# Performance work log

Measured on AMD Instinct MI355X. Metric: run time of the kernel, lower is better.

Reference implementation:

```python
import jax, jax.numpy as jnp
import numpy as np

DIM = 64
B, H, W = 4, 80, 80


def setup_inputs() -> dict:
    key = jax.random.key(0)
    k1, k2, k3 = jax.random.split(key, 3)
    x = jax.random.normal(k1, (B, DIM, H, W), dtype=jnp.float32)
    # 1x1 conv == per-pixel linear: weight [3*dim, dim], bias [3*dim]
    w_qkv = jax.random.normal(k2, (3 * DIM, DIM), dtype=jnp.float32) * (1.0 / np.sqrt(DIM).astype(np.float32))
    b_qkv = jax.random.normal(k3, (3 * DIM,), dtype=jnp.float32) * 0.01
    return {"x": x, "w_qkv": w_qkv, "b_qkv": b_qkv}


def reference(x, w_qkv, b_qkv):
    Bb, C, Hh, Ww = x.shape
    N = Hh * Ww
    # 1x1 conv -> qkv, chunked along channels
    qkv = jnp.einsum('bchw,oc->bohw', x, w_qkv) + b_qkv[None, :, None, None]
    q, k, v = jnp.split(qkv, 3, axis=1)  # each [B,C,H,W]

    # --- spatial attention (uses q on both sides, as in the original) ---
    # qk: transpose(3,1) -> [B,W,H,C] -> [B, W*H, C]
    qk = jnp.transpose(q, (0, 3, 2, 1)).reshape(Bb, N, C)
    # kq: [B, C, H*W]  (note: different flatten order than qk, faithful to source)
    kq = q.reshape(Bb, C, N)
    ms = jax.nn.softmax(jnp.matmul(qk, kq), axis=-1)  # [B, N, N]

    # --- channel attention ---
    kf = k.reshape(Bb, C, N)                                # [B, C, N]
    qf = jnp.transpose(q, (0, 3, 2, 1)).reshape(Bb, N, C)   # [B, N, C]
    ma = jax.nn.softmax(jnp.matmul(kf, qf), axis=-1)        # [B, C, C]

    # --- apply to v ---
    vq = jnp.transpose(v, (0, 3, 2, 1)).reshape(Bb, N, C)   # [B, N, C]
    ms_out = jnp.matmul(ms, vq)                             # [B, N, C]
    ms_out = jnp.swapaxes(ms_out, 1, 2).reshape(Bb, C, Hh, Ww)
    ma_out = jnp.matmul(ma, v.reshape(Bb, C, N)).reshape(Bb, C, Hh, Ww)
    return ms_out + ma_out
```

## Files before the change

kernel.cpp:

```cpp
#include <hip/hip_runtime.h>
#include <stdint.h>

#define BATCH 4
#define CH 64
#define HW 80
#define NPIX 6400
#define SPLITS 3

typedef __attribute__((ext_vector_type(8))) short bf16x8;
typedef __attribute__((ext_vector_type(4))) float f32x4;

#define QSCALE 1.2011224087864498f
#define ESHIFT 115.41560327111707f

static __device__ __forceinline__ unsigned short f2bf(float f) {
  union { float f; unsigned int u; } v; v.f = f;
  unsigned int u = v.u;
  return (unsigned short)((u + 0x7fffu + ((u >> 16) & 1u)) >> 16);
}
static __device__ __forceinline__ float bf2f(unsigned short h) {
  union { unsigned int u; float f; } v; v.u = ((unsigned int)h) << 16;
  return v.f;
}
static __device__ __forceinline__ unsigned int split_pack(float a) {
  unsigned short hi = f2bf(a);
  union { unsigned int u; float f; } hf; hf.u = ((unsigned int)hi) << 16;
  unsigned short lo = f2bf(a - hf.f);
  return (unsigned int)hi | ((unsigned int)lo << 16);
}
static __device__ __forceinline__ void deint(uint4 a, uint4 b, bf16x8* h, bf16x8* l) {
  union { unsigned int u[4]; bf16x8 v; } H, L;
  H.u[0] = __builtin_amdgcn_perm(a.y, a.x, 0x05040100u);
  H.u[1] = __builtin_amdgcn_perm(a.w, a.z, 0x05040100u);
  H.u[2] = __builtin_amdgcn_perm(b.y, b.x, 0x05040100u);
  H.u[3] = __builtin_amdgcn_perm(b.w, b.z, 0x05040100u);
  L.u[0] = __builtin_amdgcn_perm(a.y, a.x, 0x07060302u);
  L.u[1] = __builtin_amdgcn_perm(a.w, a.z, 0x07060302u);
  L.u[2] = __builtin_amdgcn_perm(b.y, b.x, 0x07060302u);
  L.u[3] = __builtin_amdgcn_perm(b.w, b.z, 0x07060302u);
  *h = H.v; *l = L.v;
}
static __device__ __forceinline__ void gload16(const unsigned short* g, char* l) {
  __builtin_amdgcn_global_load_lds(
      (const __attribute__((address_space(1))) unsigned int*)(g),
      (__attribute__((address_space(3))) unsigned int*)(l), 16, 0, 0);
}

__global__ __launch_bounds__(512) void qkv_kernel(
    const float* __restrict__ x, const float* __restrict__ w,
    const float* __restrict__ bias, unsigned short* __restrict__ Qtbf,
    unsigned short* __restrict__ Vbf, unsigned int* __restrict__ Kpk,
    unsigned int* __restrict__ Qtn) {
  __shared__ float qs[64][65];
  int bid = blockIdx.x;
  int b = bid / 100, tile = bid % 100;
  int p0 = tile * 64;
  int t = threadIdx.x;
  int i = t & 63;
  int og = __builtin_amdgcn_readfirstlane(t >> 6);
  int p = p0 + i;
  int tp = (p % HW) * HW + p / HW;
  const float* xb = x + (size_t)b * CH * NPIX + p;
  float xv[64];
#pragma unroll
  for (int c = 0; c < 64; ++c) xv[c] = xb[(size_t)c * NPIX];
  size_t bc = (size_t)b * CH * NPIX;
  for (int j = 0; j < 24; j += 4) {
    int o = og * 24 + j;
    const float* wr0 = w + o * 64;
    const float* wr1 = wr0 + 64;
    const float* wr2 = wr0 + 128;
    const float* wr3 = wr0 + 192;
    float a0 = bias[o], a1 = bias[o + 1], a2 = bias[o + 2], a3 = bias[o + 3];
#pragma unroll
    for (int c = 0; c < 64; ++c) {
      float xc = xv[c];
      a0 += wr0[c] * xc;
      a1 += wr1[c] * xc;
      a2 += wr2[c] * xc;
      a3 += wr3[c] * xc;
    }
    float av[4] = {a0, a1, a2, a3};
#pragma unroll
    for (int u = 0; u < 4; ++u) {
      int oo = o + u;
      int cc = oo & 63;
      int kind = oo >> 6;
      float a = av[u];
      if (kind == 0) {
        qs[cc][i] = a;
        Qtn[bc + (size_t)cc * NPIX + tp] = split_pack(a);
      } else if (kind == 1) {
        Kpk[bc + (size_t)cc * NPIX + p] = split_pack(a);
      } else {
        Vbf[bc + (size_t)cc * NPIX + p] = f2bf(a);
      }
    }
  }
  __syncthreads();
  int j2 = t >> 3, g = t & 7;
  int pj = p0 + j2;
  int tpj = (pj % HW) * HW + pj / HW;
  unsigned int pk4[4];
#pragma unroll
  for (int q4 = 0; q4 < 4; ++q4) {
    float a0 = qs[g * 8 + q4 * 2][j2] * QSCALE;
    float a1 = qs[g * 8 + q4 * 2 + 1][j2] * QSCALE;
    pk4[q4] = (unsigned int)f2bf(a0) | ((unsigned int)f2bf(a1) << 16);
  }
  unsigned short* dst = Qtbf + ((size_t)b * NPIX + tpj) * 64 + g * 8;
  uint4 w0 = {pk4[0], pk4[1], pk4[2], pk4[3]};
  *(uint4*)&dst[0] = w0;
}

__global__ __launch_bounds__(256) void gram_kernel(
    const unsigned int* __restrict__ Kpk, const unsigned int* __restrict__ Qtn,
    float* __restrict__ Pc) {
  int bid = blockIdx.x;
  int b = bid / 200, chunk = bid % 200;
  int n0 = chunk * 32;
  int t = threadIdx.x;
  int w = t >> 6, lane = t & 63;
  int quad = lane >> 4, l16 = lane & 15;
  size_t bc = (size_t)b * CH * NPIX;

  f32x4 acc[4];
#pragma unroll
  for (int ct = 0; ct < 4; ++ct) acc[ct] = (f32x4){0.f, 0.f, 0.f, 0.f};

  const unsigned int* kp = Kpk + bc + (size_t)(w * 16 + l16) * NPIX + n0;
  uint4 ua = *(const uint4*)&kp[quad * 8];
  uint4 ub = *(const uint4*)&kp[quad * 8 + 4];
  bf16x8 ah, al;
  deint(ua, ub, &ah, &al);
#pragma unroll
  for (int ct = 0; ct < 4; ++ct) {
    const unsigned int* qp = Qtn + bc + (size_t)(ct * 16 + l16) * NPIX + n0;
    uint4 va = *(const uint4*)&qp[quad * 8];
    uint4 vb = *(const uint4*)&qp[quad * 8 + 4];
    bf16x8 bh, bl;
    deint(va, vb, &bh, &bl);
    acc[ct] = __builtin_amdgcn_mfma_f32_16x16x32_bf16(ah, bh, acc[ct], 0, 0, 0);
    acc[ct] = __builtin_amdgcn_mfma_f32_16x16x32_bf16(ah, bl, acc[ct], 0, 0, 0);
    acc[ct] = __builtin_amdgcn_mfma_f32_16x16x32_bf16(al, bh, acc[ct], 0, 0, 0);
  }
#pragma unroll
  for (int ct = 0; ct < 4; ++ct)
#pragma unroll
    for (int r = 0; r < 4; ++r)
      atomicAdd(&Pc[((size_t)b * 64 + w * 16 + quad * 4 + r) * 64 + ct * 16 + l16],
                acc[ct][r]);
}

__global__ __launch_bounds__(256) void flash_kernel(
    const unsigned short* __restrict__ Qtbf, const unsigned short* __restrict__ Vbf,
    float* __restrict__ Opart, float* __restrict__ Lpart) {
  __shared__ char smem[40960] __attribute__((aligned(128)));

  int bid = blockIdx.x;
  int b = bid / 300;
  int rem = bid % 300;
  int qt = rem / 3, split = rem % 3;
  int p0 = qt * 64;
  int t = threadIdx.x;
  int w = t >> 6, lane = t & 63;
  int quad = lane >> 4, l16 = lane & 15;
  int sw = l16 & 7;
  size_t bq = (size_t)b * NPIX;
  size_t bC = (size_t)b * CH * NPIX;

  bf16x8 aq[2];
#pragma unroll
  for (int ks = 0; ks < 2; ++ks)
    aq[ks] = *(const bf16x8*)&Qtbf[(bq + p0 + w * 16 + l16) * 64 + ks * 32 + quad * 8];

  f32x4 oacc[4];
#pragma unroll
  for (int ct = 0; ct < 4; ++ct) oacc[ct] = (f32x4){0.f, 0.f, 0.f, 0.f};
  float psum = 0.f;

  const unsigned short* Kb = Qtbf + bq * 64;
  const unsigned short* Vb = Vbf + bC;

  int lr = lane >> 3, ls = lane & 7;
  int colsw = (ls ^ lr) * 8;
  int rA = w * 8 + lr;
  int rB = 32 + w * 8 + lr;
  int ldsA = __builtin_amdgcn_readfirstlane(w * 1024);
  int ldsB = ldsA + 4096;

  int kt0 = split * 34;
  int niter = (split == 2) ? 32 : 34;

  const unsigned short* gKA = Kb + (size_t)(kt0 * 64 + rA) * 64 + colsw;
  const unsigned short* gKB = Kb + (size_t)(kt0 * 64 + rB) * 64 + colsw;
  const unsigned short* gVA = Vb + (size_t)rA * NPIX + kt0 * 64 + colsw;
  const unsigned short* gVB = Vb + (size_t)rB * NPIX + kt0 * 64 + colsw;

  gload16(gKA, smem + ldsA);
  gload16(gKB, smem + ldsB);
  gload16(gVA, smem + 16384 + ldsA);
  gload16(gVB, smem + 16384 + ldsB);
  gKA += 64 * 64; gKB += 64 * 64; gVA += 64; gVB += 64;
  __syncthreads();

  unsigned short* Pw = (unsigned short*)(smem + 32768) + w * 16 * 64;
  for (int it = 0; it < niter; ++it) {
    int cur = it & 1;
    if (it + 1 < niter) {
      int off = (cur ^ 1) << 13;
      gload16(gKA, smem + off + ldsA);
      gload16(gKB, smem + off + ldsB);
      gload16(gVA, smem + 16384 + off + ldsA);
      gload16(gVB, smem + 16384 + off + ldsB);
      gKA += 64 * 64; gKB += 64 * 64; gVA += 64; gVB += 64;
    }
    unsigned short* Ksc = (unsigned short*)(smem + (cur << 13));
    unsigned short* Vsc = (unsigned short*)(smem + 16384 + (cur << 13));
    f32x4 sc[4];
#pragma unroll
    for (int ct = 0; ct < 4; ++ct)
      sc[ct] = (f32x4){-ESHIFT, -ESHIFT, -ESHIFT, -ESHIFT};
    __builtin_amdgcn_s_setprio(1);
#pragma unroll
    for (int ks = 0; ks < 2; ++ks)
#pragma unroll
      for (int ct = 0; ct < 4; ++ct) {
        bf16x8 bk = *(const bf16x8*)&Ksc[(ct * 16 + l16) * 64 +
                                         (((ks * 4 + quad) ^ sw) << 3)];
        sc[ct] = __builtin_amdgcn_mfma_f32_16x16x32_bf16(bk, aq[ks], sc[ct], 0, 0, 0);
      }
    __builtin_amdgcn_s_setprio(0);
#pragma unroll
    for (int ct = 0; ct < 4; ++ct) {
      float e0 = __builtin_amdgcn_exp2f(sc[ct][0]);
      float e1 = __builtin_amdgcn_exp2f(sc[ct][1]);
      float e2 = __builtin_amdgcn_exp2f(sc[ct][2]);
      float e3 = __builtin_amdgcn_exp2f(sc[ct][3]);
      psum += (e0 + e1) + (e2 + e3);
      unsigned int pk0, pk1;
      asm("v_cvt_pk_bf16_f32 %0, %1, %2" : "=v"(pk0) : "v"(e0), "v"(e1));
      asm("v_cvt_pk_bf16_f32 %0, %1, %2" : "=v"(pk1) : "v"(e2), "v"(e3));
      uint2 pk = {pk0, pk1};
      *(uint2*)&Pw[l16 * 64 +
                   (((2 * ct + (quad >> 1)) ^ sw) << 3) + ((quad & 1) << 2)] = pk;
    }
    bf16x8 pf[2];
#pragma unroll
    for (int ks = 0; ks < 2; ++ks)
      pf[ks] = *(const bf16x8*)&Pw[l16 * 64 + (((ks * 4 + quad) ^ sw) << 3)];
    __builtin_amdgcn_s_setprio(1);
#pragma unroll
    for (int ks = 0; ks < 2; ++ks)
#pragma unroll
      for (int ct = 0; ct < 4; ++ct) {
        bf16x8 vf = *(const bf16x8*)&Vsc[(ct * 16 + l16) * 64 +
                                         (((ks * 4 + quad) ^ sw) << 3)];
        oacc[ct] = __builtin_amdgcn_mfma_f32_16x16x32_bf16(vf, pf[ks], oacc[ct], 0, 0, 0);
      }
    __builtin_amdgcn_s_setprio(0);
    __syncthreads();
  }
  float* Op = Opart + (size_t)(split * BATCH + b) * CH * NPIX;
  int pcol = p0 + w * 16 + l16;
  {
    float s = psum;
    s += __shfl_xor(s, 16, 64);
    s += __shfl_xor(s, 32, 64);
    if (quad == 0) Lpart[(size_t)(split * BATCH + b) * NPIX + pcol] = s;
  }
#pragma unroll
  for (int ct = 0; ct < 4; ++ct)
#pragma unroll
    for (int r = 0; r < 4; ++r)
      Op[(size_t)(ct * 16 + quad * 4 + r) * NPIX + pcol] = oacc[ct][r];
}

__global__ __launch_bounds__(256) void finalize_kernel(
    const float* __restrict__ Pc, const unsigned short* __restrict__ Vbf,
    const float* __restrict__ Opart, const float* __restrict__ Lpart,
    float* __restrict__ out) {
  __shared__ float maT[64 * 64];
  int bid = blockIdx.x;
  int b = bid / 100, nt = bid % 100;
  int t = threadIdx.x;
  if (t < 64) {
    int c = t;
    const float* row = Pc + ((size_t)b * 64 + c) * 64;
    float v[64];
    float mx = -1e30f;
#pragma unroll
    for (int j = 0; j < 64; ++j) { v[j] = row[j]; mx = fmaxf(mx, v[j]); }
    float s = 0.f;
#pragma unroll
    for (int j = 0; j < 64; ++j) { v[j] = __expf(v[j] - mx); s += v[j]; }
    float inv = 1.f / s;
#pragma unroll
    for (int j = 0; j < 64; ++j) maT[j * 64 + c] = v[j] * inv;
  }
  __syncthreads();
  int lane = t & 63, ct = t >> 6;
  int n = nt * 64 + lane;
  size_t bc = (size_t)b * CH * NPIX;
  const unsigned short* vb = Vbf + bc + n;
  float acc[16];
#pragma unroll
  for (int j = 0; j < 16; ++j) acc[j] = 0.f;
  for (int cp = 0; cp < 64; ++cp) {
    float vv = bf2f(vb[(size_t)cp * NPIX]);
    const float* m = &maT[cp * 64 + ct * 16];
    f32x4 m0 = *(const f32x4*)&m[0];
    f32x4 m1 = *(const f32x4*)&m[4];
    f32x4 m2 = *(const f32x4*)&m[8];
    f32x4 m3 = *(const f32x4*)&m[12];
#pragma unroll
    for (int j = 0; j < 4; ++j) {
      acc[j] += m0[j] * vv;
      acc[4 + j] += m1[j] * vv;
      acc[8 + j] += m2[j] * vv;
      acc[12 + j] += m3[j] * vv;
    }
  }
  float lsum = Lpart[(size_t)(0 * BATCH + b) * NPIX + n] +
               Lpart[(size_t)(1 * BATCH + b) * NPIX + n] +
               Lpart[(size_t)(2 * BATCH + b) * NPIX + n];
  float inv = 1.f / lsum;
  const float* O0 = Opart + (size_t)(0 * BATCH + b) * CH * NPIX;
  const float* O1 = Opart + (size_t)(1 * BATCH + b) * CH * NPIX;
  const float* O2 = Opart + (size_t)(2 * BATCH + b) * CH * NPIX;
#pragma unroll
  for (int j = 0; j < 16; ++j) {
    size_t co = (size_t)(ct * 16 + j) * NPIX + n;
    float o = O0[co] + O1[co] + O2[co];
    out[bc + co] = acc[j] + o * inv;
  }
}

extern "C" void kernel_launch(void* const* d_in, const int* in_sizes, int n_in,
                              void* d_out, int out_size, void* d_ws, size_t ws_size,
                              hipStream_t stream) {
  const float* x = (const float*)d_in[0];
  const float* w = (const float*)d_in[1];
  const float* bias = (const float*)d_in[2];
  float* out = (float*)d_out;
  char* ws = (char*)d_ws;
  unsigned short* Qtbf = (unsigned short*)(ws);
  unsigned short* Vbf = (unsigned short*)(ws + 3276800);
  unsigned int* Kpk = (unsigned int*)(ws + 6553600);
  unsigned int* Qtn = (unsigned int*)(ws + 13107200);
  float* Opart = (float*)(ws + 6553600);
  float* Pc = (float*)(ws + 26214400);
  float* Lpart = (float*)(ws + 26279936);

  hipMemsetAsync(Pc, 0, 65536, stream);
  qkv_kernel<<<400, 512, 0, stream>>>(x, w, bias, Qtbf, Vbf, Kpk, Qtn);
  gram_kernel<<<800, 256, 0, stream>>>(Kpk, Qtn, Pc);
  flash_kernel<<<1200, 256, 0, stream>>>(Qtbf, Vbf, Opart, Lpart);
  finalize_kernel<<<400, 256, 0, stream>>>(Pc, Vbf, Opart, Lpart, out);
}
```

Measured before the change: 186.0 us.

## Read V directly from global in flash kernel; double gram chunk size

The flash kernel stops staging V tiles through LDS and instead loads the V MFMA fragments straight from global memory each iteration. This shrinks shared memory from 40KB to 24KB, which may allow more resident blocks. The cost is uncoalesced per-lane 16-byte global reads on the critical path with no prefetch. Separately, the gram kernel now processes 64 pixels per block instead of 32, halving the block count and the number of atomic adds.

```diff
diff --git a/kernel.cpp b/kernel.cpp
--- a/kernel.cpp
+++ b/kernel.cpp
@@ -117,8 +117,8 @@
     const unsigned int* __restrict__ Kpk, const unsigned int* __restrict__ Qtn,
     float* __restrict__ Pc) {
   int bid = blockIdx.x;
-  int b = bid / 200, chunk = bid % 200;
-  int n0 = chunk * 32;
+  int b = bid / 100, chunk = bid % 100;
+  int n0 = chunk * 64;
   int t = threadIdx.x;
   int w = t >> 6, lane = t & 63;
   int quad = lane >> 4, l16 = lane & 15;
@@ -129,20 +129,26 @@
   for (int ct = 0; ct < 4; ++ct) acc[ct] = (f32x4){0.f, 0.f, 0.f, 0.f};
 
   const unsigned int* kp = Kpk + bc + (size_t)(w * 16 + l16) * NPIX + n0;
-  uint4 ua = *(const uint4*)&kp[quad * 8];
-  uint4 ub = *(const uint4*)&kp[quad * 8 + 4];
-  bf16x8 ah, al;
-  deint(ua, ub, &ah, &al);
+  bf16x8 ah[2], al[2];
+#pragma unroll
+  for (int ks2 = 0; ks2 < 2; ++ks2) {
+    uint4 ua = *(const uint4*)&kp[ks2 * 32 + quad * 8];
+    uint4 ub = *(const uint4*)&kp[ks2 * 32 + quad * 8 + 4];
+    deint(ua, ub, &ah[ks2], &al[ks2]);
+  }
 #pragma unroll
   for (int ct = 0; ct < 4; ++ct) {
     const unsigned int* qp = Qtn + bc + (size_t)(ct * 16 + l16) * NPIX + n0;
-    uint4 va = *(const uint4*)&qp[quad * 8];
-    uint4 vb = *(const uint4*)&qp[quad * 8 + 4];
-    bf16x8 bh, bl;
-    deint(va, vb, &bh, &bl);
-    acc[ct] = __builtin_amdgcn_mfma_f32_16x16x32_bf16(ah, bh, acc[ct], 0, 0, 0);
-    acc[ct] = __builtin_amdgcn_mfma_f32_16x16x32_bf16(ah, bl, acc[ct], 0, 0, 0);
-    acc[ct] = __builtin_amdgcn_mfma_f32_16x16x32_bf16(al, bh, acc[ct], 0, 0, 0);
+#pragma unroll
+    for (int ks2 = 0; ks2 < 2; ++ks2) {
+      uint4 va = *(const uint4*)&qp[ks2 * 32 + quad * 8];
+      uint4 vb = *(const uint4*)&qp[ks2 * 32 + quad * 8 + 4];
+      bf16x8 bh, bl;
+      deint(va, vb, &bh, &bl);
+      acc[ct] = __builtin_amdgcn_mfma_f32_16x16x32_bf16(ah[ks2], bh, acc[ct], 0, 0, 0);
+      acc[ct] = __builtin_amdgcn_mfma_f32_16x16x32_bf16(ah[ks2], bl, acc[ct], 0, 0, 0);
+      acc[ct] = __builtin_amdgcn_mfma_f32_16x16x32_bf16(al[ks2], bh, acc[ct], 0, 0, 0);
+    }
   }
 #pragma unroll
   for (int ct = 0; ct < 4; ++ct)
@@ -155,7 +161,7 @@
 __global__ __launch_bounds__(256) void flash_kernel(
     const unsigned short* __restrict__ Qtbf, const unsigned short* __restrict__ Vbf,
     float* __restrict__ Opart, float* __restrict__ Lpart) {
-  __shared__ char smem[40960] __attribute__((aligned(128)));
+  __shared__ char smem[24576] __attribute__((aligned(128)));
 
   int bid = blockIdx.x;
   int b = bid / 300;
@@ -194,29 +200,23 @@
 
   const unsigned short* gKA = Kb + (size_t)(kt0 * 64 + rA) * 64 + colsw;
   const unsigned short* gKB = Kb + (size_t)(kt0 * 64 + rB) * 64 + colsw;
-  const unsigned short* gVA = Vb + (size_t)rA * NPIX + kt0 * 64 + colsw;
-  const unsigned short* gVB = Vb + (size_t)rB * NPIX + kt0 * 64 + colsw;
 
   gload16(gKA, smem + ldsA);
   gload16(gKB, smem + ldsB);
-  gload16(gVA, smem + 16384 + ldsA);
-  gload16(gVB, smem + 16384 + ldsB);
-  gKA += 64 * 64; gKB += 64 * 64; gVA += 64; gVB += 64;
+  gKA += 64 * 64; gKB += 64 * 64;
   __syncthreads();
 
-  unsigned short* Pw = (unsigned short*)(smem + 32768) + w * 16 * 64;
+  unsigned short* Pw = (unsigned short*)(smem + 16384) + w * 16 * 64;
   for (int it = 0; it < niter; ++it) {
     int cur = it & 1;
     if (it + 1 < niter) {
       int off = (cur ^ 1) << 13;
       gload16(gKA, smem + off + ldsA);
       gload16(gKB, smem + off + ldsB);
-      gload16(gVA, smem + 16384 + off + ldsA);
-      gload16(gVB, smem + 16384 + off + ldsB);
-      gKA += 64 * 64; gKB += 64 * 64; gVA += 64; gVB += 64;
+      gKA += 4096; gKB += 4096;
     }
     unsigned short* Ksc = (unsigned short*)(smem + (cur << 13));
-    unsigned short* Vsc = (unsigned short*)(smem + 16384 + (cur << 13));
+    int n0 = (kt0 + it) * 64;
     f32x4 sc[4];
 #pragma unroll
     for (int ct = 0; ct < 4; ++ct)
@@ -254,8 +254,8 @@
     for (int ks = 0; ks < 2; ++ks)
 #pragma unroll
       for (int ct = 0; ct < 4; ++ct) {
-        bf16x8 vf = *(const bf16x8*)&Vsc[(ct * 16 + l16) * 64 +
-                                         (((ks * 4 + quad) ^ sw) << 3)];
+        bf16x8 vf = *(const bf16x8*)&Vb[(size_t)(ct * 16 + l16) * NPIX + n0 +
+                                        ((ks * 4 + quad) << 3)];
         oacc[ct] = __builtin_amdgcn_mfma_f32_16x16x32_bf16(vf, pf[ks], oacc[ct], 0, 0, 0);
       }
     __builtin_amdgcn_s_setprio(0);
@@ -354,7 +354,7 @@
 
   hipMemsetAsync(Pc, 0, 65536, stream);
   qkv_kernel<<<400, 512, 0, stream>>>(x, w, bias, Qtbf, Vbf, Kpk, Qtn);
-  gram_kernel<<<800, 256, 0, stream>>>(Kpk, Qtn, Pc);
+  gram_kernel<<<400, 256, 0, stream>>>(Kpk, Qtn, Pc);
   flash_kernel<<<1200, 256, 0, stream>>>(Qtbf, Vbf, Opart, Lpart);
   finalize_kernel<<<400, 256, 0, stream>>>(Pc, Vbf, Opart, Lpart, out);
 }
```

After: 307.1 us. +65.1%, slower.
